# Kernel tuning notes

Measured on AMD Instinct MI355X. Metric: run time of the kernel, lower is better.

Reference implementation:

```python
import jax, jax.numpy as jnp
import numpy as np

USER = 100000
ITEM = 50000
N = USER + ITEM
LATDIM = 64
IMG_DIM = 1024
E_ADJ = 3_000_000
E_IMG = 1_000_000
GNN_LAYERS = 2
RIS_LAMBDA = 1.0
EPS = 1e-12


def spmm(rows, cols, vals, x):
    # sparse [N,N] @ dense [N,D] via gather + segment-sum
    return jax.ops.segment_sum(vals[:, None] * x[cols], rows, num_segments=N)


def setup_inputs() -> dict:
    key = jax.random.key(0)
    ks = jax.random.split(key, 10)
    return {
        "adj_rows": jax.random.randint(ks[0], (E_ADJ,), 0, N, dtype=jnp.int32),
        "adj_cols": jax.random.randint(ks[1], (E_ADJ,), 0, N, dtype=jnp.int32),
        "adj_vals": jax.random.uniform(ks[2], (E_ADJ,), dtype=jnp.float32),
        "img_rows": jax.random.randint(ks[3], (E_IMG,), 0, N, dtype=jnp.int32),
        "img_cols": jax.random.randint(ks[4], (E_IMG,), 0, N, dtype=jnp.int32),
        "img_vals": jax.random.uniform(ks[5], (E_IMG,), dtype=jnp.float32),
        "image_embedding": jax.random.normal(ks[6], (ITEM, IMG_DIM), dtype=jnp.float32),
        "uEmbeds": jax.random.normal(ks[7], (USER, LATDIM), dtype=jnp.float32) * 0.01,
        "iEmbeds": jax.random.normal(ks[8], (ITEM, LATDIM), dtype=jnp.float32) * 0.01,
        "W_trans": jax.random.normal(ks[9], (IMG_DIM, LATDIM), dtype=jnp.float32) * (1.0 / np.sqrt(IMG_DIM)),
        "b_trans": jnp.zeros((LATDIM,), dtype=jnp.float32),
    }


def reference(adj_rows, adj_cols, adj_vals, img_rows, img_cols, img_vals,
              image_embedding, uEmbeds, iEmbeds, W_trans, b_trans):
    # trans == 1: Linear projection of image features
    image_feats = image_embedding @ W_trans + b_trans  # [ITEM, LATDIM]

    # image_adj @ concat(u, i)
    embeds_img_adj = spmm(img_rows, img_cols, img_vals, jnp.concatenate([uEmbeds, iEmbeds], axis=0))

    # F.normalize(image_feats) along dim=1 (L2, eps=1e-12)
    nrm = jnp.linalg.norm(image_feats, axis=1, keepdims=True)
    feats_n = image_feats / jnp.maximum(nrm, EPS)

    embeds_image = spmm(adj_rows, adj_cols, adj_vals, jnp.concatenate([uEmbeds, feats_n], axis=0))
    embeds_image_ = spmm(adj_rows, adj_cols, adj_vals,
                         jnp.concatenate([embeds_image[:USER], iEmbeds], axis=0))
    embeds_image = embeds_image + embeds_image_ + RIS_LAMBDA * embeds_img_adj

    # stacked GCN layers with sum over all layer outputs (including input)
    acc = embeds_image
    cur = embeds_image
    for _ in range(GNN_LAYERS):
        cur = spmm(adj_rows, adj_cols, adj_vals, cur)
        acc = acc + cur

    return acc[:USER], acc[USER:]
```

## Files before the change

kernel.cpp:

```cpp
#include <hip/hip_runtime.h>
#include <hip/hip_fp16.h>

#define USER_N 100000
#define ITEM_N 50000
#define NN (USER_N + ITEM_N)
#define D 64
#define IMGD 1024
#define LDP 68
#define KSPLIT 4
#define KQ (IMGD / KSPLIT)

#define BUCKET_BITS 10
#define BROWS (1 << BUCKET_BITS)
#define NBUCK ((NN + BROWS - 1) >> BUCKET_BITS)
#define CHUNK 4096

typedef _Float16 v4h __attribute__((ext_vector_type(4)));
typedef _Float16 v8h __attribute__((ext_vector_type(8)));
typedef float v4f __attribute__((ext_vector_type(4)));

typedef __attribute__((address_space(1))) unsigned int GU32;
typedef __attribute__((address_space(3))) unsigned int LU32;

__global__ __launch_bounds__(256) void prep_fused(
    const float* __restrict__ uE, const float* __restrict__ iE,
    __half* __restrict__ x0, __half* __restrict__ xBI,
    const float* __restrict__ W, _Float16* __restrict__ Wt16, int cvt_blocks)
{
    if (blockIdx.x < cvt_blocks) {
        const int i = blockIdx.x * 256 + threadIdx.x;
        const int n4u = USER_N * D / 4;
        const int n4 = NN * D / 4;
        if (i >= n4) return;
        const float4 v = (i < n4u) ? reinterpret_cast<const float4*>(uE)[i]
                                   : reinterpret_cast<const float4*>(iE)[i - n4u];
        union { uint2 u2; __half2 h[2]; } o;
        o.h[0] = __floats2half2_rn(v.x, v.y);
        o.h[1] = __floats2half2_rn(v.z, v.w);
        *reinterpret_cast<uint2*>(x0 + (size_t)i * 4) = o.u2;
        if (i >= n4u)
            *reinterpret_cast<uint2*>(xBI + (size_t)(i - n4u) * 4) = o.u2;
    } else {
        const int id = (blockIdx.x - cvt_blocks) * 256 + threadIdx.x;
        if (id >= D * IMGD) return;
        const int c = id >> 10;
        const int k = id & 1023;
        Wt16[id] = (_Float16)W[(size_t)k * D + c];
    }
}

__global__ __launch_bounds__(256) void gemm_g(
    const float* __restrict__ A, const _Float16* __restrict__ Wt16,
    float* __restrict__ P0, float* __restrict__ P123,
    const int* __restrict__ rp, const int2* __restrict__ ev,
    const __half* __restrict__ src, float* __restrict__ out32,
    int gemm_blocks)
{
    __shared__ float As[32 * KQ];
    if (blockIdx.x < gemm_blocks) {
        const int t = threadIdx.x;
        const int w = t >> 6;
        const int lane = t & 63;
        const int l16 = lane & 15;
        const int g = lane >> 4;
        const int tile = blockIdx.x >> 2;
        const int ks = blockIdx.x & 3;
        const int row0 = tile * 32;
        const int kbase = ks * KQ;

#pragma unroll
        for (int i = 0; i < 8; i++) {
            const int r = w * 8 + i;
            const int grow = row0 + r;
            const int garow = grow < ITEM_N ? grow : ITEM_N - 1;
            const int xm = (r & 7) << 4;
            const char* srcp = reinterpret_cast<const char*>(
                A + (size_t)garow * IMGD + kbase) + ((lane * 16) ^ xm);
            __builtin_amdgcn_global_load_lds(
                (GU32*)srcp, (LU32*)&As[r * KQ], 16, 0, 0);
        }
        asm volatile("s_waitcnt vmcnt(0)" ::: "memory");
        __syncthreads();

        const int wr = (w >> 1) * 16;
        const int wc = (w & 1) * 32;
        const int rr = wr + l16;
        const char* rbase = reinterpret_cast<const char*>(&As[rr * KQ]);
        const int xm = (rr & 7) << 4;

        v4f acc[2] = {};
        const _Float16* wb = Wt16 + (size_t)l16 * IMGD + kbase + g * 4;

        for (int c = 0; c < KQ; c += 64) {
            const int cb = c * 4;
            const float4 f0 = *reinterpret_cast<const float4*>(rbase + ((cb + g * 16) ^ xm));
            const float4 f1 = *reinterpret_cast<const float4*>(rbase + ((cb + 64 + g * 16) ^ xm));
            const float4 f2 = *reinterpret_cast<const float4*>(rbase + ((cb + 128 + g * 16) ^ xm));
            const float4 f3 = *reinterpret_cast<const float4*>(rbase + ((cb + 192 + g * 16) ^ xm));
            union { v8h v; v4h h[2]; } af0, af1;
            {
                v4h h;
                h[0] = (_Float16)f0.x; h[1] = (_Float16)f0.y;
                h[2] = (_Float16)f0.z; h[3] = (_Float16)f0.w;
                af0.h[0] = h;
                h[0] = (_Float16)f1.x; h[1] = (_Float16)f1.y;
                h[2] = (_Float16)f1.z; h[3] = (_Float16)f1.w;
                af0.h[1] = h;
                h[0] = (_Float16)f2.x; h[1] = (_Float16)f2.y;
                h[2] = (_Float16)f2.z; h[3] = (_Float16)f2.w;
                af1.h[0] = h;
                h[0] = (_Float16)f3.x; h[1] = (_Float16)f3.y;
                h[2] = (_Float16)f3.z; h[3] = (_Float16)f3.w;
                af1.h[1] = h;
            }
#pragma unroll
            for (int n = 0; n < 2; n++) {
                const _Float16* wp = wb + (size_t)(wc + n * 16) * IMGD + c;
                union { v8h v; v4h h[2]; } bf;
                bf.h[0] = *reinterpret_cast<const v4h*>(wp);
                bf.h[1] = *reinterpret_cast<const v4h*>(wp + 16);
                acc[n] = __builtin_amdgcn_mfma_f32_16x16x32_f16(af0.v, bf.v, acc[n], 0, 0, 0);
                bf.h[0] = *reinterpret_cast<const v4h*>(wp + 32);
                bf.h[1] = *reinterpret_cast<const v4h*>(wp + 48);
                acc[n] = __builtin_amdgcn_mfma_f32_16x16x32_f16(af1.v, bf.v, acc[n], 0, 0, 0);
            }
        }
        float* Cp = (ks == 0) ? P0 : P123 + (size_t)(ks - 1) * ITEM_N * D;
#pragma unroll
        for (int n = 0; n < 2; n++) {
            const int col = wc + n * 16 + l16;
#pragma unroll
            for (int r = 0; r < 4; r++) {
                const int grow = row0 + wr + g * 4 + r;
                if (grow < ITEM_N)
                    Cp[(size_t)grow * D + col] = acc[n][r];
            }
        }
    } else {
        const int wid = ((blockIdx.x - gemm_blocks) * 256 + threadIdx.x) >> 6;
        const int lane = threadIdx.x & 63;
        const int sub = lane >> 3;
        const int l8 = lane & 7;
        const int rowbase = wid * 8;
        if (rowbase >= NN) return;
        const int row = rowbase + sub;

        int v = 0;
        if (lane <= 8 && rowbase + lane <= NN) v = rp[rowbase + lane];
        const int s = __shfl(v, sub, 64);
        const int e = __shfl(v, sub + 1, 64);

        const __half* srcl = src + l8 * 8;
        float acc[8] = {};

        union cvt4 { uint4 u; __half2 h[4]; };
        int i = s;
        for (; i + 3 < e; i += 4) {
            const int2 E0 = ev[i], E1 = ev[i + 1], E2 = ev[i + 2], E3 = ev[i + 3];
            cvt4 g0, g1, g2, g3;
            g0.u = *reinterpret_cast<const uint4*>(srcl + (size_t)E0.x * D);
            g1.u = *reinterpret_cast<const uint4*>(srcl + (size_t)E1.x * D);
            g2.u = *reinterpret_cast<const uint4*>(srcl + (size_t)E2.x * D);
            g3.u = *reinterpret_cast<const uint4*>(srcl + (size_t)E3.x * D);
#pragma unroll
            for (int k = 0; k < 4; k++) {
                const cvt4& g = k == 0 ? g0 : k == 1 ? g1 : k == 2 ? g2 : g3;
                const float w = __int_as_float(k == 0 ? E0.y : k == 1 ? E1.y
                                               : k == 2 ? E2.y : E3.y);
#pragma unroll
                for (int j = 0; j < 4; j++) {
                    const float2 f = __half22float2(g.h[j]);
                    acc[2 * j]     += w * f.x;
                    acc[2 * j + 1] += w * f.y;
                }
            }
        }
        for (; i < e; i++) {
            const int2 E0 = ev[i];
            cvt4 g;
            g.u = *reinterpret_cast<const uint4*>(srcl + (size_t)E0.x * D);
            const float w = __int_as_float(E0.y);
#pragma unroll
            for (int j = 0; j < 4; j++) {
                const float2 f = __half22float2(g.h[j]);
                acc[2 * j]     += w * f.x;
                acc[2 * j + 1] += w * f.y;
            }
        }

        if (row >= NN) return;
        const size_t idx = (size_t)row * D + l8 * 8;
#pragma unroll
        for (int h = 0; h < 2; h++) {
            float4 o;
            o.x = acc[4 * h]; o.y = acc[4 * h + 1];
            o.z = acc[4 * h + 2]; o.w = acc[4 * h + 3];
            *reinterpret_cast<float4*>(&out32[idx + h * 4]) = o;
        }
    }
}

__global__ __launch_bounds__(256) void gemm_feats32(
    const float* __restrict__ A, const float* __restrict__ W,
    const float* __restrict__ b, float* __restrict__ C)
{
    __shared__ float As[32][LDP];
    __shared__ float Ws[64][LDP];
    const int row0 = blockIdx.x * 32;
    const int t = threadIdx.x;
    const int tx = t & 15, ty = t >> 4;
    float acc[2][4] = {};

    const int lr = t >> 4;
    const int lk = (t & 15) * 4;

    for (int k0 = 0; k0 < IMGD; k0 += 64) {
#pragma unroll
        for (int i = 0; i < 2; i++) {
            const int r = lr + i * 16;
            const int grow = row0 + r;
            float4 v = make_float4(0.f, 0.f, 0.f, 0.f);
            if (grow < ITEM_N)
                v = *reinterpret_cast<const float4*>(&A[(size_t)grow * IMGD + k0 + lk]);
            *reinterpret_cast<float4*>(&As[r][lk]) = v;
        }
#pragma unroll
        for (int i = 0; i < 4; i++) {
            const int kr = lr + i * 16;
            float4 v = *reinterpret_cast<const float4*>(&W[(size_t)(k0 + kr) * D + lk]);
            *reinterpret_cast<float4*>(&Ws[kr][lk]) = v;
        }
        __syncthreads();
#pragma unroll
        for (int kb = 0; kb < 16; kb++) {
            float a_[2][4], w_[4][4];
#pragma unroll
            for (int i = 0; i < 2; i++) {
                const float4 v = *reinterpret_cast<const float4*>(&As[ty * 2 + i][kb * 4]);
                a_[i][0] = v.x; a_[i][1] = v.y; a_[i][2] = v.z; a_[i][3] = v.w;
            }
#pragma unroll
            for (int j = 0; j < 4; j++) {
                const float4 v = *reinterpret_cast<const float4*>(&Ws[kb * 4 + j][tx * 4]);
                w_[j][0] = v.x; w_[j][1] = v.y; w_[j][2] = v.z; w_[j][3] = v.w;
            }
#pragma unroll
            for (int j = 0; j < 4; j++)
#pragma unroll
                for (int i = 0; i < 2; i++)
#pragma unroll
                    for (int c = 0; c < 4; c++)
                        acc[i][c] += a_[i][j] * w_[j][c];
        }
        __syncthreads();
    }
    const float4 bias = *reinterpret_cast<const float4*>(&b[tx * 4]);
#pragma unroll
    for (int i = 0; i < 2; i++) {
        const int grow = row0 + ty * 2 + i;
        if (grow < ITEM_N) {
            float4 v;
            v.x = acc[i][0] + bias.x;
            v.y = acc[i][1] + bias.y;
            v.z = acc[i][2] + bias.z;
            v.w = acc[i][3] + bias.w;
            *reinterpret_cast<float4*>(&C[(size_t)grow * D + tx * 4]) = v;
        }
    }
}

__global__ __launch_bounds__(256) void rownorm_h4(
    const float* __restrict__ P0, const float* __restrict__ P123,
    const float* __restrict__ b, __half* __restrict__ Y, int nrows)
{
    const int gid = blockIdx.x * blockDim.x + threadIdx.x;
    const int row = gid >> 6;
    const int lane = threadIdx.x & 63;
    if (row >= nrows) return;
    const size_t idx = (size_t)row * D + lane;
    const size_t N1 = (size_t)ITEM_N * D;
    float v = P0[idx] + P123[idx] + P123[idx + N1] + P123[idx + 2 * N1] + b[lane];
    float s = v * v;
#pragma unroll
    for (int o = 32; o > 0; o >>= 1) s += __shfl_xor(s, o, 64);
    const float scale = 1.0f / fmaxf(sqrtf(s), 1e-12f);
    Y[idx] = __float2half(v * scale);
}

__global__ __launch_bounds__(256) void rownorm(float* __restrict__ X, int nrows)
{
    const int gid = blockIdx.x * blockDim.x + threadIdx.x;
    const int row = gid >> 6;
    const int lane = threadIdx.x & 63;
    if (row >= nrows) return;
    float v = X[(size_t)row * D + lane];
    float s = v * v;
#pragma unroll
    for (int o = 32; o > 0; o >>= 1) s += __shfl_xor(s, o, 64);
    const float scale = 1.0f / fmaxf(sqrtf(s), 1e-12f);
    X[(size_t)row * D + lane] = v * scale;
}

__global__ __launch_bounds__(256) void bucket_count2(
    const int* __restrict__ rows_a, int nnz_a, int nb_a, int* __restrict__ histT_a,
    const int* __restrict__ rows_b, int nnz_b, int nb_b, int* __restrict__ histT_b)
{
    const bool isA = (int)blockIdx.x < nb_a;
    const int bid = isA ? blockIdx.x : blockIdx.x - nb_a;
    const int* rows = isA ? rows_a : rows_b;
    const int nnz = isA ? nnz_a : nnz_b;
    const int nb = isA ? nb_a : nb_b;
    int* histT = isA ? histT_a : histT_b;

    __shared__ int cnt[NBUCK];
    for (int i = threadIdx.x; i < NBUCK; i += 256) cnt[i] = 0;
    __syncthreads();
    const int e0 = bid * CHUNK;
    const int e1 = min(e0 + CHUNK, nnz);
    for (int e = e0 + threadIdx.x; e < e1; e += 256)
        atomicAdd(&cnt[rows[e] >> BUCKET_BITS], 1);
    __syncthreads();
    for (int b = threadIdx.x; b < NBUCK; b += 256)
        histT[b * nb + bid] = cnt[b];
}

__global__ __launch_bounds__(1024) void scanA(
    const int* __restrict__ cnt, int* __restrict__ excl,
    int* __restrict__ blocksums, int n)
{
    const int t = threadIdx.x;
    const int gid = blockIdx.x * 1024 + t;
    const int lane = t & 63, wid = t >> 6;
    int v = (gid < n) ? cnt[gid] : 0;
    int x = v;
#pragma unroll
    for (int o = 1; o < 64; o <<= 1) {
        int y = __shfl_up(x, o, 64);
        if (lane >= o) x += y;
    }
    __shared__ int ws[16];
    __shared__ int wo[16];
    if (lane == 63) ws[wid] = x;
    __syncthreads();
    if (t < 16) {
        int s = ws[t];
        int xx = s;
#pragma unroll
        for (int o = 1; o < 16; o <<= 1) {
            int y = __shfl_up(xx, o, 16);
            if (t >= o) xx += y;
        }
        wo[t] = xx - s;
        if (t == 15) blocksums[blockIdx.x] = xx;
    }
    __syncthreads();
    if (gid < n) excl[gid] = x - v + wo[wid];
}

__global__ __launch_bounds__(1024) void scanB(int* __restrict__ bs, int nb)
{
    const int t = threadIdx.x;
    const int lane = t & 63, wid = t >> 6;
    int v = (t < nb) ? bs[t] : 0;
    int x = v;
#pragma unroll
    for (int o = 1; o < 64; o <<= 1) {
        int y = __shfl_up(x, o, 64);
        if (lane >= o) x += y;
    }
    __shared__ int ws[16];
    __shared__ int wo[16];
    if (lane == 63) ws[wid] = x;
    __syncthreads();
    if (t < 16) {
        int s = ws[t];
        int xx = s;
#pragma unroll
        for (int o = 1; o < 16; o <<= 1) {
            int y = __shfl_up(xx, o, 16);
            if (t >= o) xx += y;
        }
        wo[t] = xx - s;
    }
    __syncthreads();
    if (t < nb) bs[t] = x - v + wo[wid];
}

__global__ __launch_bounds__(256) void scan_apply(
    int* __restrict__ excl, const int* __restrict__ bo, int n)
{
    const int gid = blockIdx.x * blockDim.x + threadIdx.x;
    if (gid < n) excl[gid] += bo[gid >> 10];
}

__global__ __launch_bounds__(256) void bucket_place2(
    const int* __restrict__ rows_a, const int* __restrict__ cols_a,
    const float* __restrict__ vals_a, int nnz_a, int nb_a,
    const int* __restrict__ offsT_a, uint2* __restrict__ rec_a,
    const int* __restrict__ rows_b, const int* __restrict__ cols_b,
    const float* __restrict__ vals_b, int nnz_b, int nb_b,
    const int* __restrict__ offsT_b, uint2* __restrict__ rec_b)
{
    const bool isA = (int)blockIdx.x < nb_a;
    const int bid = isA ? blockIdx.x : blockIdx.x - nb_a;
    const int* rows = isA ? rows_a : rows_b;
    const int* cols = isA ? cols_a : cols_b;
    const float* vals = isA ? vals_a : vals_b;
    const int nnz = isA ? nnz_a : nnz_b;
    const int nb = isA ? nb_a : nb_b;
    const int* offsT = isA ? offsT_a : offsT_b;
    uint2* rec = isA ? rec_a : rec_b;

    __shared__ int cur[NBUCK];
    for (int b = threadIdx.x; b < NBUCK; b += 256)
        cur[b] = offsT[b * nb + bid];
    __syncthreads();
    const int e0 = bid * CHUNK;
    const int e1 = min(e0 + CHUNK, nnz);
    for (int e = e0 + threadIdx.x; e < e1; e += 256) {
        const int r = rows[e];
        const int b = r >> BUCKET_BITS;
        const int pos = atomicAdd(&cur[b], 1);
        rec[pos] = make_uint2(((unsigned)cols[e] << BUCKET_BITS) |
                                  (unsigned)(r & (BROWS - 1)),
                              __float_as_uint(vals[e]));
    }
}

__global__ __launch_bounds__(1024) void bucket_finalize2(
    const uint2* __restrict__ rec_a, int nnz_a, int nb_a,
    const int* __restrict__ offsT_a, int* __restrict__ rp_a, int2* __restrict__ ev_a,
    const uint2* __restrict__ rec_b, int nnz_b, int nb_b,
    const int* __restrict__ offsT_b, int* __restrict__ rp_b, int2* __restrict__ ev_b)
{
    const bool isA = (int)blockIdx.x < NBUCK;
    const int b = isA ? blockIdx.x : blockIdx.x - NBUCK;
    const uint2* rec = isA ? rec_a : rec_b;
    const int nnz = isA ? nnz_a : nnz_b;
    const int nb = isA ? nb_a : nb_b;
    const int* offsT = isA ? offsT_a : offsT_b;
    int* rp = isA ? rp_a : rp_b;
    int2* ev = isA ? ev_a : ev_b;

    const int t = threadIdx.x;
    const int rlo = b << BUCKET_BITS;
    const int segs = offsT[b * nb];
    const int sege = (b + 1 < NBUCK) ? offsT[(b + 1) * nb] : nnz;

    __shared__ int cnt[BROWS];
    __shared__ int cur[BROWS];
    cnt[t] = 0;
    __syncthreads();
    for (int i = segs + t; i < sege; i += 1024)
        atomicAdd(&cnt[rec[i].x & (BROWS - 1)], 1);
    __syncthreads();

    const int lane = t & 63, wid = t >> 6;
    const int v = cnt[t];
    int x = v;
#pragma unroll
    for (int o = 1; o < 64; o <<= 1) {
        int y = __shfl_up(x, o, 64);
        if (lane >= o) x += y;
    }
    __shared__ int wsum[16];
    __shared__ int woff[16];
    if (lane == 63) wsum[wid] = x;
    __syncthreads();
    if (t < 16) {
        int s = wsum[t];
        int xx = s;
#pragma unroll
        for (int o = 1; o < 16; o <<= 1) {
            int y = __shfl_up(xx, o, 16);
            if (t >= o) xx += y;
        }
        woff[t] = xx - s;
    }
    __syncthreads();
    const int start = segs + (x - v + woff[wid]);

    if (rlo + t < NN) rp[rlo + t] = start;
    if (b == NBUCK - 1 && t == 0) rp[NN] = nnz;
    cur[t] = start;
    __syncthreads();

    for (int i = segs + t; i < sege; i += 1024) {
        const uint2 R = rec[i];
        const int rl = (int)(R.x & (BROWS - 1));
        const int c = (int)(R.x >> BUCKET_BITS);
        const int pos = atomicAdd(&cur[rl], 1);
        ev[pos] = make_int2(c, (int)R.y);
    }
}

__global__ __launch_bounds__(256) void spmm_h8(
    const int* __restrict__ rp, const int2* __restrict__ ev,
    const __half* __restrict__ src,
    float* __restrict__ out32, __half* __restrict__ out16, int limit16,
    const float* __restrict__ add1, const float* __restrict__ add2)
{
    const int wid = (blockIdx.x * 256 + threadIdx.x) >> 6;
    const int lane = threadIdx.x & 63;
    const int sub = lane >> 3;
    const int l8 = lane & 7;
    const int rowbase = wid * 8;
    if (rowbase >= NN) return;
    const int row = rowbase + sub;

    int v = 0;
    if (lane <= 8 && rowbase + lane <= NN) v = rp[rowbase + lane];
    const int s = __shfl(v, sub, 64);
    const int e = __shfl(v, sub + 1, 64);

    const __half* srcl = src + l8 * 8;
    float acc[8] = {};

    union cvt4 { uint4 u; __half2 h[4]; };
    int i = s;
    for (; i + 3 < e; i += 4) {
        const int2 E0 = ev[i], E1 = ev[i + 1], E2 = ev[i + 2], E3 = ev[i + 3];
        cvt4 g0, g1, g2, g3;
        g0.u = *reinterpret_cast<const uint4*>(srcl + (size_t)E0.x * D);
        g1.u = *reinterpret_cast<const uint4*>(srcl + (size_t)E1.x * D);
        g2.u = *reinterpret_cast<const uint4*>(srcl + (size_t)E2.x * D);
        g3.u = *reinterpret_cast<const uint4*>(srcl + (size_t)E3.x * D);
#pragma unroll
        for (int k = 0; k < 4; k++) {
            const cvt4& g = k == 0 ? g0 : k == 1 ? g1 : k == 2 ? g2 : g3;
            const float w = __int_as_float(k == 0 ? E0.y : k == 1 ? E1.y
                                           : k == 2 ? E2.y : E3.y);
#pragma unroll
            for (int j = 0; j < 4; j++) {
                const float2 f = __half22float2(g.h[j]);
                acc[2 * j]     += w * f.x;
                acc[2 * j + 1] += w * f.y;
            }
        }
    }
    for (; i < e; i++) {
        const int2 E0 = ev[i];
        cvt4 g;
        g.u = *reinterpret_cast<const uint4*>(srcl + (size_t)E0.x * D);
        const float w = __int_as_float(E0.y);
#pragma unroll
        for (int j = 0; j < 4; j++) {
            const float2 f = __half22float2(g.h[j]);
            acc[2 * j]     += w * f.x;
            acc[2 * j + 1] += w * f.y;
        }
    }

    if (row >= NN) return;
    const size_t idx = (size_t)row * D + l8 * 8;
#pragma unroll
    for (int h = 0; h < 2; h++) {
        if (add1) {
            const float4 a = *reinterpret_cast<const float4*>(&add1[idx + h * 4]);
            acc[4 * h] += a.x; acc[4 * h + 1] += a.y;
            acc[4 * h + 2] += a.z; acc[4 * h + 3] += a.w;
        }
        if (add2) {
            const float4 a = *reinterpret_cast<const float4*>(&add2[idx + h * 4]);
            acc[4 * h] += a.x; acc[4 * h + 1] += a.y;
            acc[4 * h + 2] += a.z; acc[4 * h + 3] += a.w;
        }
        float4 o;
        o.x = acc[4 * h]; o.y = acc[4 * h + 1];
        o.z = acc[4 * h + 2]; o.w = acc[4 * h + 3];
        *reinterpret_cast<float4*>(&out32[idx + h * 4]) = o;
    }
    if (row < limit16) {
        cvt4 o16;
#pragma unroll
        for (int j = 0; j < 4; j++)
            o16.h[j] = __floats2half2_rn(acc[2 * j], acc[2 * j + 1]);
        *reinterpret_cast<uint4*>(&out16[idx]) = o16.u;
    }
}

__global__ __launch_bounds__(256) void spmm_csr(
    const int* __restrict__ rp, const int2* __restrict__ ev,
    const float* __restrict__ srcU, const float* __restrict__ srcI,
    float* __restrict__ out,
    const float* __restrict__ add1, const float* __restrict__ add2)
{
    const int gid = blockIdx.x * blockDim.x + threadIdx.x;
    const int row = gid >> 6;
    const int lane = threadIdx.x & 63;
    if (row >= NN) return;
    const int s = rp[row], e = rp[row + 1];
    float acc = 0.f;
    int i = s;
    for (; i + 3 < e; i += 4) {
        const int2 e0 = ev[i], e1 = ev[i + 1], e2 = ev[i + 2], e3 = ev[i + 3];
        const float* p0 = (e0.x < USER_N) ? (srcU + (size_t)e0.x * D)
                                          : (srcI + (size_t)(e0.x - USER_N) * D);
        const float* p1 = (e1.x < USER_N) ? (srcU + (size_t)e1.x * D)
                                          : (srcI + (size_t)(e1.x - USER_N) * D);
        const float* p2 = (e2.x < USER_N) ? (srcU + (size_t)e2.x * D)
                                          : (srcI + (size_t)(e2.x - USER_N) * D);
        const float* p3 = (e3.x < USER_N) ? (srcU + (size_t)e3.x * D)
                                          : (srcI + (size_t)(e3.x - USER_N) * D);
        acc += __int_as_float(e0.y) * p0[lane];
        acc += __int_as_float(e1.y) * p1[lane];
        acc += __int_as_float(e2.y) * p2[lane];
        acc += __int_as_float(e3.y) * p3[lane];
    }
    for (; i < e; i++) {
        const int2 e0 = ev[i];
        const float* p0 = (e0.x < USER_N) ? (srcU + (size_t)e0.x * D)
                                          : (srcI + (size_t)(e0.x - USER_N) * D);
        acc += __int_as_float(e0.y) * p0[lane];
    }
    const size_t idx = (size_t)row * D + lane;
    if (add1) acc += add1[idx];
    if (add2) acc += add2[idx];
    out[idx] = acc;
}

extern "C" void kernel_launch(void* const* d_in, const int* in_sizes, int n_in,
                              void* d_out, int out_size, void* d_ws, size_t ws_size,
                              hipStream_t stream)
{
    const int*   adj_rows = (const int*)d_in[0];
    const int*   adj_cols = (const int*)d_in[1];
    const float* adj_vals = (const float*)d_in[2];
    const int*   img_rows = (const int*)d_in[3];
    const int*   img_cols = (const int*)d_in[4];
    const float* img_vals = (const float*)d_in[5];
    const float* img_emb  = (const float*)d_in[6];
    const float* uEmb     = (const float*)d_in[7];
    const float* iEmb     = (const float*)d_in[8];
    const float* Wt       = (const float*)d_in[9];
    const float* bt       = (const float*)d_in[10];
    float* out = (float*)d_out;

    const int e_adj = in_sizes[0];
    const int e_img = in_sizes[3];
    const int e_max = e_adj > e_img ? e_adj : e_img;
    const int NB_adj = (e_adj + CHUNK - 1) / CHUNK;
    const int NB_img = (e_img + CHUNK - 1) / CHUNK;

    const size_t ndbytes = (size_t)NN * D * sizeof(float);
    const size_t nhbytes = (size_t)NN * D * sizeof(__half);

    size_t off = 0;
    auto carve = [&](size_t bytes) { size_t p = off; off += (bytes + 255) & ~(size_t)255; return p; };
    char* base = (char*)d_ws;
    const size_t o_featsN = carve((size_t)ITEM_N * D * sizeof(float));
    const size_t o_bufA   = carve(ndbytes);
    const size_t o_bufB   = carve(ndbytes);
    const size_t o_rpAdj  = carve((NN + 1) * sizeof(int));
    const size_t o_rpImg  = carve((NN + 1) * sizeof(int));
    const size_t o_bsums  = carve(1024 * sizeof(int));
    const size_t o_histTA = carve((size_t)NBUCK * NB_adj * sizeof(int));
    const size_t o_histTB = carve((size_t)NBUCK * NB_img * sizeof(int));
    const size_t o_recA   = carve((size_t)e_max * sizeof(uint2) > nhbytes
                                      ? (size_t)e_max * sizeof(uint2) : nhbytes);
    const size_t o_evAdj  = carve((size_t)e_adj * sizeof(int2));
    const size_t need_base = off;
    const size_t o_evImg  = carve((size_t)e_img * sizeof(int2) > nhbytes
                                      ? (size_t)e_img * sizeof(int2) : nhbytes);
    const size_t o_x0     = carve((size_t)e_img * sizeof(uint2) > nhbytes
                                      ? (size_t)e_img * sizeof(uint2) : nhbytes);
    const size_t o_wt16   = carve((size_t)D * IMGD * sizeof(_Float16));
    const size_t need_h = off;

    if (ws_size < need_base) return;
    const bool use_h = (ws_size >= need_h);

    float* featsN = (float*)(base + o_featsN);
    float* bufA   = (float*)(base + o_bufA);
    float* bufB   = (float*)(base + o_bufB);
    int* rpAdj    = (int*)(base + o_rpAdj);
    int* rpImg    = (int*)(base + o_rpImg);
    int* bsums    = (int*)(base + o_bsums);
    int* histTA   = (int*)(base + o_histTA);
    int* histTB   = (int*)(base + o_histTB);
    uint2* recA   = (uint2*)(base + o_recA);
    uint2* recB   = (uint2*)(base + o_x0);
    int2* evAdj   = (int2*)(base + o_evAdj);
    int2* evImg   = (int2*)(base + o_evImg);
    __half* xC    = (__half*)(base + o_recA);
    __half* xB    = (__half*)(base + o_evImg);
    __half* x0    = (__half*)(base + o_x0);
    _Float16* wt16 = (_Float16*)(base + o_wt16);

    const int SPMM8_GRID = (NN + 31) / 32;
    const int SPMM_GRID = (NN * 64 + 255) / 256;
    const int RN_GRID = (ITEM_N * 64 + 255) / 256;
    const int GEMM_BLOCKS = ((ITEM_N + 31) / 32) * KSPLIT;

    if (use_h) {
        __half* x0I = x0 + (size_t)USER_N * D;
        __half* xBI = xB + (size_t)USER_N * D;

        bucket_count2<<<NB_adj + NB_img, 256, 0, stream>>>(
            adj_rows, e_adj, NB_adj, histTA, img_rows, e_img, NB_img, histTB);
        {
            const int nA = NBUCK * NB_adj, nsbA = (nA + 1023) / 1024;
            scanA<<<nsbA, 1024, 0, stream>>>(histTA, histTA, bsums, nA);
            scanB<<<1, 1024, 0, stream>>>(bsums, nsbA);
            scan_apply<<<(nA + 255) / 256, 256, 0, stream>>>(histTA, bsums, nA);
            const int nB = NBUCK * NB_img, nsbB = (nB + 1023) / 1024;
            scanA<<<nsbB, 1024, 0, stream>>>(histTB, histTB, bsums, nB);
            scanB<<<1, 1024, 0, stream>>>(bsums, nsbB);
            scan_apply<<<(nB + 255) / 256, 256, 0, stream>>>(histTB, bsums, nB);
        }
        bucket_place2<<<NB_adj + NB_img, 256, 0, stream>>>(
            adj_rows, adj_cols, adj_vals, e_adj, NB_adj, histTA, recA,
            img_rows, img_cols, img_vals, e_img, NB_img, histTB, recB);
        bucket_finalize2<<<2 * NBUCK, 1024, 0, stream>>>(
            recA, e_adj, NB_adj, histTA, rpAdj, evAdj,
            recB, e_img, NB_img, histTB, rpImg, evImg);

        const int CVT_BLOCKS = (NN * D / 4 + 255) / 256;
        prep_fused<<<CVT_BLOCKS + (D * IMGD + 255) / 256, 256, 0, stream>>>(
            uEmb, iEmb, x0, xBI, Wt, wt16, CVT_BLOCKS);

        gemm_g<<<GEMM_BLOCKS + SPMM8_GRID, 256, 0, stream>>>(
            img_emb, wt16, featsN, bufB, rpImg, evImg, x0, bufA, GEMM_BLOCKS);

        rownorm_h4<<<RN_GRID, 256, 0, stream>>>(featsN, bufB, bt, x0I, ITEM_N);

        spmm_h8<<<SPMM8_GRID, 256, 0, stream>>>(
            rpAdj, evAdj, x0, bufB, xB, USER_N, nullptr, nullptr);

        spmm_h8<<<SPMM8_GRID, 256, 0, stream>>>(
            rpAdj, evAdj, xB, bufA, xC, NN, bufB, bufA);

        spmm_h8<<<SPMM8_GRID, 256, 0, stream>>>(
            rpAdj, evAdj, xC, bufB, x0, NN, nullptr, nullptr);

        spmm_h8<<<SPMM8_GRID, 256, 0, stream>>>(
            rpAdj, evAdj, x0, out, nullptr, 0, bufA, bufB);
    } else {
        bucket_count2<<<NB_adj + NB_img, 256, 0, stream>>>(
            adj_rows, e_adj, NB_adj, histTA, img_rows, e_img, NB_img, histTB);
        {
            const int nA = NBUCK * NB_adj, nsbA = (nA + 1023) / 1024;
            scanA<<<nsbA, 1024, 0, stream>>>(histTA, histTA, bsums, nA);
            scanB<<<1, 1024, 0, stream>>>(bsums, nsbA);
            scan_apply<<<(nA + 255) / 256, 256, 0, stream>>>(histTA, bsums, nA);
            const int nB = NBUCK * NB_img, nsbB = (nB + 1023) / 1024;
            scanA<<<nsbB, 1024, 0, stream>>>(histTB, histTB, bsums, nB);
            scanB<<<1, 1024, 0, stream>>>(bsums, nsbB);
            scan_apply<<<(nB + 255) / 256, 256, 0, stream>>>(histTB, bsums, nB);
        }
        bucket_place2<<<NB_adj + NB_img, 256, 0, stream>>>(
            adj_rows, adj_cols, adj_vals, e_adj, NB_adj, histTA, recA,
            img_rows, img_cols, img_vals, e_img, NB_img, histTB, recB);
        bucket_finalize2<<<2 * NBUCK, 1024, 0, stream>>>(
            recA, e_adj, NB_adj, histTA, rpAdj, evAdj,
            recB, e_img, NB_img, histTB, rpImg, evImg);

        gemm_feats32<<<(ITEM_N + 31) / 32, 256, 0, stream>>>(img_emb, Wt, bt, featsN);
        rownorm<<<RN_GRID, 256, 0, stream>>>(featsN, ITEM_N);

        spmm_csr<<<SPMM_GRID, 256, 0, stream>>>(
            rpImg, evImg, uEmb, iEmb, bufA, nullptr, nullptr);
        spmm_csr<<<SPMM_GRID, 256, 0, stream>>>(
            rpAdj, evAdj, uEmb, featsN, bufB, nullptr, nullptr);
        spmm_csr<<<SPMM_GRID, 256, 0, stream>>>(
            rpAdj, evAdj, bufB, iEmb, bufA, bufB, bufA);
        spmm_csr<<<SPMM_GRID, 256, 0, stream>>>(
            rpAdj, evAdj, bufA, bufA + (size_t)USER_N * D, bufB, nullptr, nullptr);
        spmm_csr<<<SPMM_GRID, 256, 0, stream>>>(
            rpAdj, evAdj, bufB, bufB + (size_t)USER_N * D, out, bufA, bufB);
    }
}
```

Baseline: 565.1 us.

## Phase SpMM gathers by column range, interleave GEMM/SpMM blocks, merge scan launches

Each SpMM row is now walked six times, and each pass only gathers source rows whose column index falls in one 25000-row window. The aim is to keep the gathered working set resident in L2/MALL. The fused GEMM+SpMM launch now interleaves blocks 4:3 so both workloads are co-resident, and the A/B scan kernels are merged into single launches with separate block-sum buffers. The phasing re-reads the edge list six times and adds divergent predicated branches, which risks extra memory traffic and ALU work.

```diff
diff --git a/kernel.cpp b/kernel.cpp
--- a/kernel.cpp
+++ b/kernel.cpp
@@ -14,6 +14,9 @@
 #define BROWS (1 << BUCKET_BITS)
 #define NBUCK ((NN + BROWS - 1) >> BUCKET_BITS)
 #define CHUNK 4096
+
+#define PHASES 6
+#define CPH 25000
 
 typedef _Float16 v4h __attribute__((ext_vector_type(4)));
 typedef _Float16 v8h __attribute__((ext_vector_type(8)));
@@ -54,17 +57,20 @@
     float* __restrict__ P0, float* __restrict__ P123,
     const int* __restrict__ rp, const int2* __restrict__ ev,
     const __half* __restrict__ src, float* __restrict__ out32,
-    int gemm_blocks)
+    int gemm_blocks, int g_blocks)
 {
     __shared__ float As[32 * KQ];
-    if (blockIdx.x < gemm_blocks) {
+    const int q = blockIdx.x / 7, r7 = blockIdx.x % 7;
+    if (r7 < 4) {
+        const int gb = q * 4 + r7;
+        if (gb >= gemm_blocks) return;
         const int t = threadIdx.x;
         const int w = t >> 6;
         const int lane = t & 63;
         const int l16 = lane & 15;
         const int g = lane >> 4;
-        const int tile = blockIdx.x >> 2;
-        const int ks = blockIdx.x & 3;
+        const int tile = gb >> 2;
+        const int ks = gb & 3;
         const int row0 = tile * 32;
         const int kbase = ks * KQ;
 
@@ -137,7 +143,9 @@
             }
         }
     } else {
-        const int wid = ((blockIdx.x - gemm_blocks) * 256 + threadIdx.x) >> 6;
+        const int sb = q * 3 + (r7 - 4);
+        if (sb >= g_blocks) return;
+        const int wid = (sb * 256 + threadIdx.x) >> 6;
         const int lane = threadIdx.x & 63;
         const int sub = lane >> 3;
         const int l8 = lane & 7;
@@ -324,12 +332,18 @@
         histT[b * nb + bid] = cnt[b];
 }
 
-__global__ __launch_bounds__(1024) void scanA(
-    const int* __restrict__ cnt, int* __restrict__ excl,
-    int* __restrict__ blocksums, int n)
-{
+__global__ __launch_bounds__(1024) void scanA2(
+    int* __restrict__ histTA, int* __restrict__ bsumsA, int nA, int nsbA,
+    int* __restrict__ histTB, int* __restrict__ bsumsB, int nB)
+{
+    const bool isA = (int)blockIdx.x < nsbA;
+    int* cnt = isA ? histTA : histTB;
+    int* bsums = isA ? bsumsA : bsumsB;
+    const int n = isA ? nA : nB;
+    const int bid = isA ? blockIdx.x : blockIdx.x - nsbA;
+
     const int t = threadIdx.x;
-    const int gid = blockIdx.x * 1024 + t;
+    const int gid = bid * 1024 + t;
     const int lane = t & 63, wid = t >> 6;
     int v = (gid < n) ? cnt[gid] : 0;
     int x = v;
@@ -351,14 +365,17 @@
             if (t >= o) xx += y;
         }
         wo[t] = xx - s;
-        if (t == 15) blocksums[blockIdx.x] = xx;
-    }
-    __syncthreads();
-    if (gid < n) excl[gid] = x - v + wo[wid];
-}
-
-__global__ __launch_bounds__(1024) void scanB(int* __restrict__ bs, int nb)
-{
+        if (t == 15) bsums[bid] = xx;
+    }
+    __syncthreads();
+    if (gid < n) cnt[gid] = x - v + wo[wid];
+}
+
+__global__ __launch_bounds__(1024) void scanB2(
+    int* __restrict__ bsA, int nbA, int* __restrict__ bsB, int nbB)
+{
+    int* bs = blockIdx.x == 0 ? bsA : bsB;
+    const int nb = blockIdx.x == 0 ? nbA : nbB;
     const int t = threadIdx.x;
     const int lane = t & 63, wid = t >> 6;
     int v = (t < nb) ? bs[t] : 0;
@@ -386,11 +403,13 @@
     if (t < nb) bs[t] = x - v + wo[wid];
 }
 
-__global__ __launch_bounds__(256) void scan_apply(
-    int* __restrict__ excl, const int* __restrict__ bo, int n)
+__global__ __launch_bounds__(256) void scan_apply2(
+    int* __restrict__ histTA, const int* __restrict__ bsA, int nA,
+    int* __restrict__ histTB, const int* __restrict__ bsB, int nB)
 {
     const int gid = blockIdx.x * blockDim.x + threadIdx.x;
-    if (gid < n) excl[gid] += bo[gid >> 10];
+    if (gid < nA) histTA[gid] += bsA[gid >> 10];
+    else if (gid - nA < nB) histTB[gid - nA] += bsB[(gid - nA) >> 10];
 }
 
 __global__ __launch_bounds__(256) void bucket_place2(
@@ -494,7 +513,7 @@
     }
 }
 
-__global__ __launch_bounds__(256) void spmm_h8(
+__global__ __launch_bounds__(256) void spmm_h8p(
     const int* __restrict__ rp, const int2* __restrict__ ev,
     const __half* __restrict__ src,
     float* __restrict__ out32, __half* __restrict__ out16, int limit16,
@@ -517,37 +536,66 @@
     float acc[8] = {};
 
     union cvt4 { uint4 u; __half2 h[4]; };
-    int i = s;
-    for (; i + 3 < e; i += 4) {
-        const int2 E0 = ev[i], E1 = ev[i + 1], E2 = ev[i + 2], E3 = ev[i + 3];
-        cvt4 g0, g1, g2, g3;
-        g0.u = *reinterpret_cast<const uint4*>(srcl + (size_t)E0.x * D);
-        g1.u = *reinterpret_cast<const uint4*>(srcl + (size_t)E1.x * D);
-        g2.u = *reinterpret_cast<const uint4*>(srcl + (size_t)E2.x * D);
-        g3.u = *reinterpret_cast<const uint4*>(srcl + (size_t)E3.x * D);
-#pragma unroll
-        for (int k = 0; k < 4; k++) {
-            const cvt4& g = k == 0 ? g0 : k == 1 ? g1 : k == 2 ? g2 : g3;
-            const float w = __int_as_float(k == 0 ? E0.y : k == 1 ? E1.y
-                                           : k == 2 ? E2.y : E3.y);
-#pragma unroll
-            for (int j = 0; j < 4; j++) {
-                const float2 f = __half22float2(g.h[j]);
-                acc[2 * j]     += w * f.x;
-                acc[2 * j + 1] += w * f.y;
-            }
-        }
-    }
-    for (; i < e; i++) {
-        const int2 E0 = ev[i];
-        cvt4 g;
-        g.u = *reinterpret_cast<const uint4*>(srcl + (size_t)E0.x * D);
-        const float w = __int_as_float(E0.y);
-#pragma unroll
-        for (int j = 0; j < 4; j++) {
-            const float2 f = __half22float2(g.h[j]);
-            acc[2 * j]     += w * f.x;
-            acc[2 * j + 1] += w * f.y;
+#pragma unroll 1
+    for (int p = 0; p < PHASES; p++) {
+        const unsigned lo = (unsigned)(p * CPH);
+        int i = s;
+        for (; i + 3 < e; i += 4) {
+            const int2 E0 = ev[i], E1 = ev[i + 1], E2 = ev[i + 2], E3 = ev[i + 3];
+            const bool m0 = (unsigned)E0.x - lo < (unsigned)CPH;
+            const bool m1 = (unsigned)E1.x - lo < (unsigned)CPH;
+            const bool m2 = (unsigned)E2.x - lo < (unsigned)CPH;
+            const bool m3 = (unsigned)E3.x - lo < (unsigned)CPH;
+            cvt4 g0, g1, g2, g3;
+            if (m0) g0.u = *reinterpret_cast<const uint4*>(srcl + (size_t)E0.x * D);
+            if (m1) g1.u = *reinterpret_cast<const uint4*>(srcl + (size_t)E1.x * D);
+            if (m2) g2.u = *reinterpret_cast<const uint4*>(srcl + (size_t)E2.x * D);
+            if (m3) g3.u = *reinterpret_cast<const uint4*>(srcl + (size_t)E3.x * D);
+            if (m0) {
+                const float w = __int_as_float(E0.y);
+#pragma unroll
+                for (int j = 0; j < 4; j++) {
+                    const float2 f = __half22float2(g0.h[j]);
+                    acc[2 * j] += w * f.x; acc[2 * j + 1] += w * f.y;
+                }
+            }
+            if (m1) {
+                const float w = __int_as_float(E1.y);
+#pragma unroll
+                for (int j = 0; j < 4; j++) {
+                    const float2 f = __half22float2(g1.h[j]);
+                    acc[2 * j] += w * f.x; acc[2 * j + 1] += w * f.y;
+                }
+            }
+            if (m2) {
+                const float w = __int_as_float(E2.y);
+#pragma unroll
+                for (int j = 0; j < 4; j++) {
+                    const float2 f = __half22float2(g2.h[j]);
+                    acc[2 * j] += w * f.x; acc[2 * j + 1] += w * f.y;
+                }
+            }
+            if (m3) {
+                const float w = __int_as_float(E3.y);
+#pragma unroll
+                for (int j = 0; j < 4; j++) {
+                    const float2 f = __half22float2(g3.h[j]);
+                    acc[2 * j] += w * f.x; acc[2 * j + 1] += w * f.y;
+                }
+            }
+        }
+        for (; i < e; i++) {
+            const int2 E0 = ev[i];
+            if ((unsigned)E0.x - lo < (unsigned)CPH) {
+                cvt4 g;
+                g.u = *reinterpret_cast<const uint4*>(srcl + (size_t)E0.x * D);
+                const float w = __int_as_float(E0.y);
+#pragma unroll
+                for (int j = 0; j < 4; j++) {
+                    const float2 f = __half22float2(g.h[j]);
+                    acc[2 * j] += w * f.x; acc[2 * j + 1] += w * f.y;
+                }
+            }
         }
     }
 
@@ -653,7 +701,8 @@
     const size_t o_bufB   = carve(ndbytes);
     const size_t o_rpAdj  = carve((NN + 1) * sizeof(int));
     const size_t o_rpImg  = carve((NN + 1) * sizeof(int));
-    const size_t o_bsums  = carve(1024 * sizeof(int));
+    const size_t o_bsumsA = carve(1024 * sizeof(int));
+    const size_t o_bsumsB = carve(1024 * sizeof(int));
     const size_t o_histTA = carve((size_t)NBUCK * NB_adj * sizeof(int));
     const size_t o_histTB = carve((size_t)NBUCK * NB_img * sizeof(int));
     const size_t o_recA   = carve((size_t)e_max * sizeof(uint2) > nhbytes
@@ -675,7 +724,8 @@
     float* bufB   = (float*)(base + o_bufB);
     int* rpAdj    = (int*)(base + o_rpAdj);
     int* rpImg    = (int*)(base + o_rpImg);
-    int* bsums    = (int*)(base + o_bsums);
+    int* bsumsA   = (int*)(base + o_bsumsA);
+    int* bsumsB   = (int*)(base + o_bsumsB);
     int* histTA   = (int*)(base + o_histTA);
     int* histTB   = (int*)(base + o_histTB);
     uint2* recA   = (uint2*)(base + o_recA);
@@ -691,70 +741,50 @@
     const int SPMM_GRID = (NN * 64 + 255) / 256;
     const int RN_GRID = (ITEM_N * 64 + 255) / 256;
     const int GEMM_BLOCKS = ((ITEM_N + 31) / 32) * KSPLIT;
+    const int MEGA_GRID = 1563 * 7;
+
+    const int nA = NBUCK * NB_adj, nsbA = (nA + 1023) / 1024;
+    const int nB = NBUCK * NB_img, nsbB = (nB + 1023) / 1024;
+    bucket_count2<<<NB_adj + NB_img, 256, 0, stream>>>(
+        adj_rows, e_adj, NB_adj, histTA, img_rows, e_img, NB_img, histTB);
+    scanA2<<<nsbA + nsbB, 1024, 0, stream>>>(
+        histTA, bsumsA, nA, nsbA, histTB, bsumsB, nB);
+    scanB2<<<2, 1024, 0, stream>>>(bsumsA, nsbA, bsumsB, nsbB);
+    scan_apply2<<<(nA + nB + 255) / 256, 256, 0, stream>>>(
+        histTA, bsumsA, nA, histTB, bsumsB, nB);
+    bucket_place2<<<NB_adj + NB_img, 256, 0, stream>>>(
+        adj_rows, adj_cols, adj_vals, e_adj, NB_adj, histTA, recA,
+        img_rows, img_cols, img_vals, e_img, NB_img, histTB, recB);
+    bucket_finalize2<<<2 * NBUCK, 1024, 0, stream>>>(
+        recA, e_adj, NB_adj, histTA, rpAdj, evAdj,
+        recB, e_img, NB_img, histTB, rpImg, evImg);
 
     if (use_h) {
         __half* x0I = x0 + (size_t)USER_N * D;
         __half* xBI = xB + (size_t)USER_N * D;
 
-        bucket_count2<<<NB_adj + NB_img, 256, 0, stream>>>(
-            adj_rows, e_adj, NB_adj, histTA, img_rows, e_img, NB_img, histTB);
-        {
-            const int nA = NBUCK * NB_adj, nsbA = (nA + 1023) / 1024;
-            scanA<<<nsbA, 1024, 0, stream>>>(histTA, histTA, bsums, nA);
-            scanB<<<1, 1024, 0, stream>>>(bsums, nsbA);
-            scan_apply<<<(nA + 255) / 256, 256, 0, stream>>>(histTA, bsums, nA);
-            const int nB = NBUCK * NB_img, nsbB = (nB + 1023) / 1024;
-            scanA<<<nsbB, 1024, 0, stream>>>(histTB, histTB, bsums, nB);
-            scanB<<<1, 1024, 0, stream>>>(bsums, nsbB);
-            scan_apply<<<(nB + 255) / 256, 256, 0, stream>>>(histTB, bsums, nB);
-        }
-        bucket_place2<<<NB_adj + NB_img, 256, 0, stream>>>(
-            adj_rows, adj_cols, adj_vals, e_adj, NB_adj, histTA, recA,
-            img_rows, img_cols, img_vals, e_img, NB_img, histTB, recB);
-        bucket_finalize2<<<2 * NBUCK, 1024, 0, stream>>>(
-            recA, e_adj, NB_adj, histTA, rpAdj, evAdj,
-            recB, e_img, NB_img, histTB, rpImg, evImg);
-
         const int CVT_BLOCKS = (NN * D / 4 + 255) / 256;
         prep_fused<<<CVT_BLOCKS + (D * IMGD + 255) / 256, 256, 0, stream>>>(
             uEmb, iEmb, x0, xBI, Wt, wt16, CVT_BLOCKS);
 
-        gemm_g<<<GEMM_BLOCKS + SPMM8_GRID, 256, 0, stream>>>(
-            img_emb, wt16, featsN, bufB, rpImg, evImg, x0, bufA, GEMM_BLOCKS);
+        gemm_g<<<MEGA_GRID, 256, 0, stream>>>(
+            img_emb, wt16, featsN, bufB, rpImg, evImg, x0, bufA,
+            GEMM_BLOCKS, SPMM8_GRID);
 
         rownorm_h4<<<RN_GRID, 256, 0, stream>>>(featsN, bufB, bt, x0I, ITEM_N);
 
-        spmm_h8<<<SPMM8_GRID, 256, 0, stream>>>(
+        spmm_h8p<<<SPMM8_GRID, 256, 0, stream>>>(
             rpAdj, evAdj, x0, bufB, xB, USER_N, nullptr, nullptr);
 
-        spmm_h8<<<SPMM8_GRID, 256, 0, stream>>>(
+        spmm_h8p<<<SPMM8_GRID, 256, 0, stream>>>(
             rpAdj, evAdj, xB, bufA, xC, NN, bufB, bufA);
 
-        spmm_h8<<<SPMM8_GRID, 256, 0, stream>>>(
+        spmm_h8p<<<SPMM8_GRID, 256, 0, stream>>>(
             rpAdj, evAdj, xC, bufB, x0, NN, nullptr, nullptr);
 
-        spmm_h8<<<SPMM8_GRID, 256, 0, stream>>>(
+        spmm_h8p<<<SPMM8_GRID, 256, 0, stream>>>(
             rpAdj, evAdj, x0, out, nullptr, 0, bufA, bufB);
     } else {
-        bucket_count2<<<NB_adj + NB_img, 256, 0, stream>>>(
-            adj_rows, e_adj, NB_adj, histTA, img_rows, e_img, NB_img, histTB);
-        {
-            const int nA = NBUCK * NB_adj, nsbA = (nA + 1023) / 1024;
-            scanA<<<nsbA, 1024, 0, stream>>>(histTA, histTA, bsums, nA);
-            scanB<<<1, 1024, 0, stream>>>(bsums, nsbA);
-            scan_apply<<<(nA + 255) / 256, 256, 0, stream>>>(histTA, bsums, nA);
-            const int nB = NBUCK * NB_img, nsbB = (nB + 1023) / 1024;
-            scanA<<<nsbB, 1024, 0, stream>>>(histTB, histTB, bsums, nB);
-            scanB<<<1, 1024, 0, stream>>>(bsums, nsbB);
-            scan_apply<<<(nB + 255) / 256, 256, 0, stream>>>(histTB, bsums, nB);
-        }
-        bucket_place2<<<NB_adj + NB_img, 256, 0, stream>>>(
-            adj_rows, adj_cols, adj_vals, e_adj, NB_adj, histTA, recA,
-            img_rows, img_cols, img_vals, e_img, NB_img, histTB, recB);
-        bucket_finalize2<<<2 * NBUCK, 1024, 0, stream>>>(
-            recA, e_adj, NB_adj, histTA, rpAdj, evAdj,
-            recB, e_img, NB_img, histTB, rpImg, evImg);
-
         gemm_feats32<<<(ITEM_N + 31) / 32, 256, 0, stream>>>(img_emb, Wt, bt, featsN);
         rownorm<<<RN_GRID, 256, 0, stream>>>(featsN, ITEM_N);
 
```

After: 941.9 us. +66.7%, slower.
